# Kernel tuning notes

Hardware: AMD Instinct MI355X
Metric: run time of the kernel (lower is better)

## Reference

```python
import jax, jax.numpy as jnp
import numpy as np

B, T, D, H = 2, 2048, 2048, 16
HD = D // H
SCALE = HD ** -0.5
NEG_INF = float('-inf')


def setup_inputs() -> dict:
    key = jax.random.key(0)
    ks = jax.random.split(key, 10)
    x = jax.random.normal(ks[0], (B, T, D), dtype=jnp.float32)
    # causal float mask: 0 on/below diagonal, -inf above (broadcast over B, H)
    causal = jnp.triu(jnp.ones((T, T), dtype=bool), k=1)
    mask = jnp.where(causal, NEG_INF, 0.0).astype(jnp.float32)[None, None]
    # xavier_uniform for [D, D]: bound = sqrt(6 / (D + D))
    bound = float(np.sqrt(6.0 / (D + D)))
    def xav(k):
        return jax.random.uniform(k, (D, D), jnp.float32, -bound, bound)
    wq, wk, wv, wo = xav(ks[1]), xav(ks[2]), xav(ks[3]), xav(ks[4])
    # biases: uniform_[0,1)
    bq = jax.random.uniform(ks[5], (D,), jnp.float32)
    bk = jax.random.uniform(ks[6], (D,), jnp.float32)
    bv = jax.random.uniform(ks[7], (D,), jnp.float32)
    bo = jax.random.uniform(ks[8], (D,), jnp.float32)
    return {"x": x, "mask": mask, "wq": wq, "bq": bq, "wk": wk, "bk": bk,
            "wv": wv, "bv": bv, "wo": wo, "bo": bo}


def reference(x, mask, wq, bq, wk, bk, wv, bv, wo, bo):
    b, t, d = x.shape
    def split_heads(y):  # [B,T,D] -> [B,H,T,HD]
        return y.reshape(b, t, H, HD).transpose(0, 2, 1, 3)
    q = split_heads(x @ wq.T + bq)
    k = split_heads(x @ wk.T + bk)
    v = split_heads(x @ wv.T + bv)
    scores = jnp.einsum('bhqd,bhkd->bhqk', q, k) * SCALE
    scores = jnp.where(mask == NEG_INF, NEG_INF, scores)
    attn = jax.nn.softmax(scores, axis=-1)
    out = jnp.einsum('bhqk,bhkd->bhqd', attn, v)  # [B,H,T,HD]
    out = out.transpose(0, 2, 1, 3).reshape(b, t, d)
    return out @ wo.T + bo
```

## Files before the change

### kernel.cpp

```cpp
#include <hip/hip_runtime.h>

typedef unsigned short u16;
typedef __bf16 bf16x8 __attribute__((ext_vector_type(8)));
typedef float f32x4 __attribute__((ext_vector_type(4)));

constexpr int B_ = 2, T_ = 2048, D_ = 2048, H_ = 16, HD_ = 128;
constexpr int MROWS = B_ * T_;
constexpr int KD = D_;
constexpr int ND = D_;
#define SL2E (0.08838834764831845f * 1.4426950408889634f)

__device__ __forceinline__ u16 f2bf(float f) {
  unsigned u = __float_as_uint(f);
  u += 0x7FFF + ((u >> 16) & 1);
  return (u16)(u >> 16);
}

__device__ __forceinline__ float fexp2(float x) { return __builtin_amdgcn_exp2f(x); }

__device__ __forceinline__ void async16(const void* g, void* l) {
  __builtin_amdgcn_global_load_lds((__attribute__((address_space(1))) void*)g,
                                   (__attribute__((address_space(3))) void*)l,
                                   16, 0, 0);
}

__global__ void cvt6_kernel(const float* __restrict__ x,
                            const float* __restrict__ w0, const float* __restrict__ w1,
                            const float* __restrict__ w2, const float* __restrict__ w3,
                            u16* __restrict__ xo,
                            u16* __restrict__ o0, u16* __restrict__ o1,
                            u16* __restrict__ o2, u16* __restrict__ o3) {
  const int y = blockIdx.y;
  const float* in = y == 0 ? x : y == 1 ? x + 4194304 :
                    y == 2 ? w0 : y == 3 ? w1 : y == 4 ? w2 : w3;
  u16* out = y == 0 ? xo : y == 1 ? xo + 4194304 :
             y == 2 ? o0 : y == 3 ? o1 : y == 4 ? o2 : o3;
  const int i = (blockIdx.x * blockDim.x + threadIdx.x) * 4;
  const float4 v = *(const float4*)(in + i);
  ushort4 h;
  h.x = f2bf(v.x); h.y = f2bf(v.y); h.z = f2bf(v.z); h.w = f2bf(v.w);
  *(ushort4*)(out + i) = h;
}

template <int MODE>
__device__ __forceinline__ void gemm_body(const u16* __restrict__ A,
                                          const u16* __restrict__ Bw,
                                          const float* __restrict__ bias,
                                          void* __restrict__ outp,
                                          u16* As, u16* Bs) {
  constexpr int BK = 32;
  const int tid = threadIdx.x;
  const int wave = tid >> 6;
  const int lane = tid & 63;
  const int quad = lane >> 4;
  const int l16 = lane & 15;
  const int wm = (wave >> 1) * 64;
  const int wn = (wave & 1) * 64;
  const int mBase = blockIdx.y * 128;
  const int nBase = blockIdx.x * 128;

  f32x4 acc[4][4] = {};

  const int srow = wave * 32 + (lane >> 2);
  const int soff = ((lane & 3) ^ ((lane >> 3) & 3)) * 8;
  const u16* Ag = A + (size_t)(mBase + srow) * KD + soff;
  const u16* Bg = Bw + (size_t)(nBase + srow) * KD + soff;
  u16* AsW0 = &As[(wave * 32) * BK];
  u16* AsW1 = &As[(wave * 32 + 16) * BK];
  u16* BsW0 = &Bs[(wave * 32) * BK];
  u16* BsW1 = &Bs[(wave * 32 + 16) * BK];

  const int sw = (quad ^ ((l16 >> 1) & 3)) * 8;

  for (int k0 = 0; k0 < KD; k0 += BK) {
    __syncthreads();
    async16(Ag + k0, AsW0);
    async16(Ag + 16 * KD + k0, AsW1);
    async16(Bg + k0, BsW0);
    async16(Bg + 16 * KD + k0, BsW1);
    __syncthreads();

    bf16x8 a[4], b[4];
#pragma unroll
    for (int i = 0; i < 4; i++)
      a[i] = *(const bf16x8*)&As[(wm + i * 16 + l16) * BK + sw];
#pragma unroll
    for (int j = 0; j < 4; j++)
      b[j] = *(const bf16x8*)&Bs[(wn + j * 16 + l16) * BK + sw];
#pragma unroll
    for (int i = 0; i < 4; i++)
#pragma unroll
      for (int j = 0; j < 4; j++)
        acc[i][j] = __builtin_amdgcn_mfma_f32_16x16x32_bf16(a[i], b[j], acc[i][j], 0, 0, 0);
  }

  float* outF = (float*)outp;
  u16* outH = (u16*)outp;
#pragma unroll
  for (int i = 0; i < 4; i++) {
#pragma unroll
    for (int j = 0; j < 4; j++) {
      const int col = nBase + wn + j * 16 + l16;
      const float bv = bias[col];
#pragma unroll
      for (int r = 0; r < 4; r++) {
        const int row = mBase + wm + i * 16 + quad * 4 + r;
        const float v = acc[i][j][r] + bv;
        if (MODE == 0) {
          outH[(size_t)row * ND + col] = f2bf(v);
        } else if (MODE == 1) {
          const int bb = row >> 11;
          const int t = row & (T_ - 1);
          const int h = col >> 7;
          const int d = col & (HD_ - 1);
          outH[(size_t)(((bb * H_ + h) << 7) + d) * T_ + t] = f2bf(v);
        } else {
          outF[(size_t)row * ND + col] = v;
        }
      }
    }
  }
}

__global__ __launch_bounds__(256) void gemm_qkv(const u16* __restrict__ A,
                                                const u16* __restrict__ Wq, const u16* __restrict__ Wk,
                                                const u16* __restrict__ Wv,
                                                const float* __restrict__ bq, const float* __restrict__ bk,
                                                const float* __restrict__ bv,
                                                u16* __restrict__ Qo, u16* __restrict__ Ko,
                                                u16* __restrict__ Vo) {
  __shared__ u16 As[128 * 32];
  __shared__ u16 Bs[128 * 32];
  const int z = blockIdx.z;
  const u16* Bw = z == 0 ? Wq : z == 1 ? Wk : Wv;
  const float* bias = z == 0 ? bq : z == 1 ? bk : bv;
  if (z == 2)
    gemm_body<1>(A, Bw, bias, (void*)Vo, As, Bs);
  else
    gemm_body<0>(A, Bw, bias, (void*)(z == 0 ? Qo : Ko), As, Bs);
}

__global__ __launch_bounds__(256) void gemm_out(const u16* __restrict__ A, const u16* __restrict__ Bw,
                                                const float* __restrict__ bias, float* __restrict__ outp) {
  __shared__ u16 As[128 * 32];
  __shared__ u16 Bs[128 * 32];
  gemm_body<2>(A, Bw, bias, (void*)outp, As, Bs);
}

constexpr int PSTR = 72;

__global__ __launch_bounds__(256, 2) void attn_kernel(const u16* __restrict__ Q,
                                                      const u16* __restrict__ Kc,
                                                      const u16* __restrict__ Vt,
                                                      u16* __restrict__ O) {
  __shared__ u16 Ks[2][64 * 128];
  __shared__ u16 Vs[2][128 * 64];
  __shared__ u16 Ps[4 * 16 * PSTR];
  const int tid = threadIdx.x;
  const int wave = tid >> 6;
  const int lane = tid & 63;
  const int quad = lane >> 4;
  const int l16 = lane & 15;
  const int lo = blockIdx.x;
  const int hi = 31 - lo;
  const int bh = blockIdx.y;
  const int b = bh >> 4;
  const int h = bh & 15;

  const int tIdx[2] = {lo, hi};

  bf16x8 qf[2][4];
#pragma unroll
  for (int t = 0; t < 2; t++) {
    const u16* Qp = Q + (size_t)(b * T_ + tIdx[t] * 64 + wave * 16 + l16) * D_ + h * HD_;
#pragma unroll
    for (int kc = 0; kc < 4; kc++)
      qf[t][kc] = *(const bf16x8*)(Qp + kc * 32 + quad * 8);
  }

  f32x4 o[2][8] = {};
  float mrow[2], lrow[2];
#pragma unroll
  for (int t = 0; t < 2; t++) { mrow[t] = -__builtin_huge_valf(); lrow[t] = 0.f; }

  const u16* Kg = Kc + (size_t)(b * T_) * D_ + h * HD_;
  const u16* Vg = Vt + (size_t)((b * H_ + h) * HD_) * T_;
  u16* Pw = &Ps[wave * 16 * PSTR];
  const int swz = (l16 & 7);

  const u16* kgp[4];
  int klo[4];
  const u16* vgp[4];
  int vlo[4];
#pragma unroll
  for (int c = 0; c < 4; c++) {
    const int krl = wave * 16 + c * 4 + (lane >> 4);
    const int kch = (lane & 15) ^ (krl & 7);
    kgp[c] = Kg + (size_t)krl * D_ + kch * 8;
    klo[c] = (wave * 16 + c * 4) * 128;
    const int vrl = wave * 32 + c * 8 + (lane >> 3);
    const int vch = (lane & 7) ^ (vrl & 7);
    vgp[c] = Vg + (size_t)vrl * T_ + vch * 8;
    vlo[c] = (wave * 32 + c * 8) * 64;
  }

#pragma unroll
  for (int c = 0; c < 4; c++) async16(kgp[c], &Ks[0][klo[c]]);
#pragma unroll
  for (int c = 0; c < 4; c++) async16(vgp[c], &Vs[0][vlo[c]]);

  for (int kt = 0; kt <= hi; kt++) {
    const int cur = kt & 1;
    __syncthreads();

    if (kt < hi) {
      const int nxt = cur ^ 1;
#pragma unroll
      for (int c = 0; c < 4; c++) async16(kgp[c] + (size_t)(kt + 1) * 64 * D_, &Ks[nxt][klo[c]]);
#pragma unroll
      for (int c = 0; c < 4; c++) async16(vgp[c] + (size_t)(kt + 1) * 64, &Vs[nxt][vlo[c]]);
    }

#pragma unroll
    for (int t = 0; t < 2; t++) {
      if (t == 0 && kt > lo) continue;

      f32x4 st[4];
#pragma unroll
      for (int nt = 0; nt < 4; nt++) {
        f32x4 a = {};
#pragma unroll
        for (int kc = 0; kc < 4; kc++) {
          const int pos = (kc * 4 + quad) ^ swz;
          bf16x8 kf = *(const bf16x8*)&Ks[cur][(nt * 16 + l16) * 128 + pos * 8];
          a = __builtin_amdgcn_mfma_f32_16x16x32_bf16(kf, qf[t][kc], a, 0, 0, 0);
        }
        st[nt] = a;
      }

      const bool diag = (kt == tIdx[t]);
#pragma unroll
      for (int nt = 0; nt < 4; nt++)
#pragma unroll
        for (int r = 0; r < 4; r++) {
          float v = st[nt][r] * SL2E;
          if (diag) {
            const int kcol = nt * 16 + quad * 4 + r;
            const int qrow = wave * 16 + l16;
            if (kcol > qrow) v = -__builtin_huge_valf();
          }
          st[nt][r] = v;
        }

      float mx = st[0][0];
#pragma unroll
      for (int nt = 0; nt < 4; nt++)
#pragma unroll
        for (int r = 0; r < 4; r++) mx = fmaxf(mx, st[nt][r]);
      mx = fmaxf(mx, __shfl_xor(mx, 16));
      mx = fmaxf(mx, __shfl_xor(mx, 32));

      if (__all(mx - mrow[t] <= 8.0f)) {
        const float mold = mrow[t];
        float sum = 0.f;
#pragma unroll
        for (int nt = 0; nt < 4; nt++)
#pragma unroll
          for (int r = 0; r < 4; r++) {
            const float p = fexp2(st[nt][r] - mold);
            st[nt][r] = p;
            sum += p;
          }
        lrow[t] += sum;
      } else {
        const float mnew = fmaxf(mrow[t], mx);
        const float alpha = fexp2(mrow[t] - mnew);
        mrow[t] = mnew;
        float sum = 0.f;
#pragma unroll
        for (int nt = 0; nt < 4; nt++)
#pragma unroll
          for (int r = 0; r < 4; r++) {
            const float p = fexp2(st[nt][r] - mnew);
            st[nt][r] = p;
            sum += p;
          }
        lrow[t] = lrow[t] * alpha + sum;

        float af[4];
#pragma unroll
        for (int r = 0; r < 4; r++) af[r] = __shfl(alpha, quad * 4 + r);
#pragma unroll
        for (int dt = 0; dt < 8; dt++)
#pragma unroll
          for (int r = 0; r < 4; r++)
            o[t][dt][r] *= af[r];
      }

#pragma unroll
      for (int nt = 0; nt < 4; nt++) {
        ushort4 pk;
        pk.x = f2bf(st[nt][0]); pk.y = f2bf(st[nt][1]);
        pk.z = f2bf(st[nt][2]); pk.w = f2bf(st[nt][3]);
        *(ushort4*)&Pw[l16 * PSTR + nt * 16 + quad * 4] = pk;
      }

      bf16x8 pf[2];
#pragma unroll
      for (int kc = 0; kc < 2; kc++)
        pf[kc] = *(const bf16x8*)&Pw[l16 * PSTR + kc * 32 + quad * 8];
#pragma unroll
      for (int dt = 0; dt < 8; dt++) {
#pragma unroll
        for (int kc = 0; kc < 2; kc++) {
          const int pos = (kc * 4 + quad) ^ swz;
          bf16x8 vf = *(const bf16x8*)&Vs[cur][(dt * 16 + l16) * 64 + pos * 8];
          o[t][dt] = __builtin_amdgcn_mfma_f32_16x16x32_bf16(pf[kc], vf, o[t][dt], 0, 0, 0);
        }
      }
    }
  }

#pragma unroll
  for (int t = 0; t < 2; t++) {
    float ltot = lrow[t];
    ltot += __shfl_xor(ltot, 16);
    ltot += __shfl_xor(ltot, 32);
    float linv[4];
#pragma unroll
    for (int r = 0; r < 4; r++) linv[r] = 1.f / __shfl(ltot, quad * 4 + r);
#pragma unroll
    for (int dt = 0; dt < 8; dt++)
#pragma unroll
      for (int r = 0; r < 4; r++) {
        const int rowg = b * T_ + tIdx[t] * 64 + wave * 16 + quad * 4 + r;
        const int col = h * HD_ + dt * 16 + l16;
        O[(size_t)rowg * D_ + col] = f2bf(o[t][dt][r] * linv[r]);
      }
  }
}

extern "C" void kernel_launch(void* const* d_in, const int* in_sizes, int n_in,
                              void* d_out, int out_size, void* d_ws, size_t ws_size,
                              hipStream_t stream) {
  (void)in_sizes; (void)n_in; (void)out_size; (void)ws_size;
  const float* x  = (const float*)d_in[0];
  const float* wq = (const float*)d_in[2];
  const float* bq = (const float*)d_in[3];
  const float* wk = (const float*)d_in[4];
  const float* bk = (const float*)d_in[5];
  const float* wv = (const float*)d_in[6];
  const float* bv = (const float*)d_in[7];
  const float* wo = (const float*)d_in[8];
  const float* bo = (const float*)d_in[9];

  u16* ws  = (u16*)d_ws;
  u16* xb  = ws;
  u16* wqb = ws + 8388608;
  u16* wkb = ws + 12582912;
  u16* wvb = ws + 16777216;
  u16* wob = ws + 20971520;
  u16* Qb  = ws + 25165824;
  u16* Kb  = ws + 33554432;
  u16* Vtb = ws + 41943040;
  u16* Ob  = ws + 50331648;

  cvt6_kernel<<<dim3(4096, 6), 256, 0, stream>>>(x, wq, wk, wv, wo,
                                                 xb, wqb, wkb, wvb, wob);

  dim3 gg(ND / 128, MROWS / 128, 3);
  gemm_qkv<<<gg, 256, 0, stream>>>(xb, wqb, wkb, wvb, bq, bk, bv, Qb, Kb, Vtb);
  attn_kernel<<<dim3(16, B_ * H_), 256, 0, stream>>>(Qb, Kb, Vtb, Ob);
  gemm_out<<<dim3(ND / 128, MROWS / 128), 256, 0, stream>>>(Ob, wob, bo, (float*)d_out);
}
```

Measured before the change: 391.1 us.

## Assign contiguous 128-row query tiles per block and share K/V fragments

Replaces the balanced lo/hi pairing of two 64-row query tiles with one contiguous 128-row query tile per block. Each wave now handles two 16-row query groups against the same K and V fragments, so each LDS fragment load feeds two MFMAs. The block loops over 2p+2 key tiles and masks causally by absolute position on the last two. This roughly halves K/V traffic per block, but the work per block becomes uneven. Blocks range from 2 to 32 key tiles, each doing two groups, so the longest block may run longer than under the old balanced pairing.

```diff
diff --git a/kernel.cpp b/kernel.cpp
--- a/kernel.cpp
+++ b/kernel.cpp
@@ -161,27 +161,25 @@
   const int lane = tid & 63;
   const int quad = lane >> 4;
   const int l16 = lane & 15;
-  const int lo = blockIdx.x;
-  const int hi = 31 - lo;
+  const int p = 15 - blockIdx.x;
   const int bh = blockIdx.y;
   const int b = bh >> 4;
   const int h = bh & 15;
-
-  const int tIdx[2] = {lo, hi};
+  const int nkt = 2 * p + 2;
 
   bf16x8 qf[2][4];
 #pragma unroll
-  for (int t = 0; t < 2; t++) {
-    const u16* Qp = Q + (size_t)(b * T_ + tIdx[t] * 64 + wave * 16 + l16) * D_ + h * HD_;
+  for (int qg = 0; qg < 2; qg++) {
+    const u16* Qp = Q + (size_t)(b * T_ + p * 128 + wave * 32 + qg * 16 + l16) * D_ + h * HD_;
 #pragma unroll
     for (int kc = 0; kc < 4; kc++)
-      qf[t][kc] = *(const bf16x8*)(Qp + kc * 32 + quad * 8);
+      qf[qg][kc] = *(const bf16x8*)(Qp + kc * 32 + quad * 8);
   }
 
   f32x4 o[2][8] = {};
   float mrow[2], lrow[2];
 #pragma unroll
-  for (int t = 0; t < 2; t++) { mrow[t] = -__builtin_huge_valf(); lrow[t] = 0.f; }
+  for (int qg = 0; qg < 2; qg++) { mrow[qg] = -__builtin_huge_valf(); lrow[qg] = 0.f; }
 
   const u16* Kg = Kc + (size_t)(b * T_) * D_ + h * HD_;
   const u16* Vg = Vt + (size_t)((b * H_ + h) * HD_) * T_;
@@ -209,11 +207,11 @@
 #pragma unroll
   for (int c = 0; c < 4; c++) async16(vgp[c], &Vs[0][vlo[c]]);
 
-  for (int kt = 0; kt <= hi; kt++) {
+  for (int kt = 0; kt < nkt; kt++) {
     const int cur = kt & 1;
     __syncthreads();
 
-    if (kt < hi) {
+    if (kt + 1 < nkt) {
       const int nxt = cur ^ 1;
 #pragma unroll
       for (int c = 0; c < 4; c++) async16(kgp[c] + (size_t)(kt + 1) * 64 * D_, &Ks[nxt][klo[c]]);
@@ -221,71 +219,77 @@
       for (int c = 0; c < 4; c++) async16(vgp[c] + (size_t)(kt + 1) * 64, &Vs[nxt][vlo[c]]);
     }
 
-#pragma unroll
-    for (int t = 0; t < 2; t++) {
-      if (t == 0 && kt > lo) continue;
-
-      f32x4 st[4];
-#pragma unroll
-      for (int nt = 0; nt < 4; nt++) {
-        f32x4 a = {};
-#pragma unroll
-        for (int kc = 0; kc < 4; kc++) {
-          const int pos = (kc * 4 + quad) ^ swz;
-          bf16x8 kf = *(const bf16x8*)&Ks[cur][(nt * 16 + l16) * 128 + pos * 8];
-          a = __builtin_amdgcn_mfma_f32_16x16x32_bf16(kf, qf[t][kc], a, 0, 0, 0);
-        }
-        st[nt] = a;
-      }
-
-      const bool diag = (kt == tIdx[t]);
+    f32x4 st[2][4];
+#pragma unroll
+    for (int nt = 0; nt < 4; nt++) {
+      bf16x8 kf[4];
+#pragma unroll
+      for (int kc = 0; kc < 4; kc++) {
+        const int pos = (kc * 4 + quad) ^ swz;
+        kf[kc] = *(const bf16x8*)&Ks[cur][(nt * 16 + l16) * 128 + pos * 8];
+      }
+      f32x4 a0 = {}, a1 = {};
+#pragma unroll
+      for (int kc = 0; kc < 4; kc++)
+        a0 = __builtin_amdgcn_mfma_f32_16x16x32_bf16(kf[kc], qf[0][kc], a0, 0, 0, 0);
+#pragma unroll
+      for (int kc = 0; kc < 4; kc++)
+        a1 = __builtin_amdgcn_mfma_f32_16x16x32_bf16(kf[kc], qf[1][kc], a1, 0, 0, 0);
+      st[0][nt] = a0;
+      st[1][nt] = a1;
+    }
+
+    const bool diag = (kt >= 2 * p);
+    bf16x8 pf[2][2];
+#pragma unroll
+    for (int qg = 0; qg < 2; qg++) {
 #pragma unroll
       for (int nt = 0; nt < 4; nt++)
 #pragma unroll
         for (int r = 0; r < 4; r++) {
-          float v = st[nt][r] * SL2E;
+          float v = st[qg][nt][r] * SL2E;
           if (diag) {
-            const int kcol = nt * 16 + quad * 4 + r;
-            const int qrow = wave * 16 + l16;
+            const int kcol = kt * 64 + nt * 16 + quad * 4 + r;
+            const int qrow = p * 128 + wave * 32 + qg * 16 + l16;
             if (kcol > qrow) v = -__builtin_huge_valf();
           }
-          st[nt][r] = v;
+          st[qg][nt][r] = v;
         }
 
-      float mx = st[0][0];
+      float mx = st[qg][0][0];
 #pragma unroll
       for (int nt = 0; nt < 4; nt++)
 #pragma unroll
-        for (int r = 0; r < 4; r++) mx = fmaxf(mx, st[nt][r]);
+        for (int r = 0; r < 4; r++) mx = fmaxf(mx, st[qg][nt][r]);
       mx = fmaxf(mx, __shfl_xor(mx, 16));
       mx = fmaxf(mx, __shfl_xor(mx, 32));
 
-      if (__all(mx - mrow[t] <= 8.0f)) {
-        const float mold = mrow[t];
+      if (__all(mx - mrow[qg] <= 8.0f)) {
+        const float mold = mrow[qg];
         float sum = 0.f;
 #pragma unroll
         for (int nt = 0; nt < 4; nt++)
 #pragma unroll
           for (int r = 0; r < 4; r++) {
-            const float p = fexp2(st[nt][r] - mold);
-            st[nt][r] = p;
-            sum += p;
+            const float pv = fexp2(st[qg][nt][r] - mold);
+            st[qg][nt][r] = pv;
+            sum += pv;
           }
-        lrow[t] += sum;
+        lrow[qg] += sum;
       } else {
-        const float mnew = fmaxf(mrow[t], mx);
-        const float alpha = fexp2(mrow[t] - mnew);
-        mrow[t] = mnew;
+        const float mnew = fmaxf(mrow[qg], mx);
+        const float alpha = fexp2(mrow[qg] - mnew);
+        mrow[qg] = mnew;
         float sum = 0.f;
 #pragma unroll
         for (int nt = 0; nt < 4; nt++)
 #pragma unroll
           for (int r = 0; r < 4; r++) {
-            const float p = fexp2(st[nt][r] - mnew);
-            st[nt][r] = p;
-            sum += p;
+            const float pv = fexp2(st[qg][nt][r] - mnew);
+            st[qg][nt][r] = pv;
+            sum += pv;
           }
-        lrow[t] = lrow[t] * alpha + sum;
+        lrow[qg] = lrow[qg] * alpha + sum;
 
         float af[4];
 #pragma unroll
@@ -294,36 +298,36 @@
         for (int dt = 0; dt < 8; dt++)
 #pragma unroll
           for (int r = 0; r < 4; r++)
-            o[t][dt][r] *= af[r];
+            o[qg][dt][r] *= af[r];
       }
 
 #pragma unroll
       for (int nt = 0; nt < 4; nt++) {
         ushort4 pk;
-        pk.x = f2bf(st[nt][0]); pk.y = f2bf(st[nt][1]);
-        pk.z = f2bf(st[nt][2]); pk.w = f2bf(st[nt][3]);
+        pk.x = f2bf(st[qg][nt][0]); pk.y = f2bf(st[qg][nt][1]);
+        pk.z = f2bf(st[qg][nt][2]); pk.w = f2bf(st[qg][nt][3]);
         *(ushort4*)&Pw[l16 * PSTR + nt * 16 + quad * 4] = pk;
       }
-
-      bf16x8 pf[2];
 #pragma unroll
       for (int kc = 0; kc < 2; kc++)
-        pf[kc] = *(const bf16x8*)&Pw[l16 * PSTR + kc * 32 + quad * 8];
-#pragma unroll
-      for (int dt = 0; dt < 8; dt++) {
-#pragma unroll
-        for (int kc = 0; kc < 2; kc++) {
-          const int pos = (kc * 4 + quad) ^ swz;
-          bf16x8 vf = *(const bf16x8*)&Vs[cur][(dt * 16 + l16) * 64 + pos * 8];
-          o[t][dt] = __builtin_amdgcn_mfma_f32_16x16x32_bf16(pf[kc], vf, o[t][dt], 0, 0, 0);
-        }
-      }
-    }
-  }
-
-#pragma unroll
-  for (int t = 0; t < 2; t++) {
-    float ltot = lrow[t];
+        pf[qg][kc] = *(const bf16x8*)&Pw[l16 * PSTR + kc * 32 + quad * 8];
+    }
+
+#pragma unroll
+    for (int dt = 0; dt < 8; dt++) {
+#pragma unroll
+      for (int kc = 0; kc < 2; kc++) {
+        const int pos = (kc * 4 + quad) ^ swz;
+        bf16x8 vf = *(const bf16x8*)&Vs[cur][(dt * 16 + l16) * 64 + pos * 8];
+        o[0][dt] = __builtin_amdgcn_mfma_f32_16x16x32_bf16(pf[0][kc], vf, o[0][dt], 0, 0, 0);
+        o[1][dt] = __builtin_amdgcn_mfma_f32_16x16x32_bf16(pf[1][kc], vf, o[1][dt], 0, 0, 0);
+      }
+    }
+  }
+
+#pragma unroll
+  for (int qg = 0; qg < 2; qg++) {
+    float ltot = lrow[qg];
     ltot += __shfl_xor(ltot, 16);
     ltot += __shfl_xor(ltot, 32);
     float linv[4];
@@ -333,9 +337,9 @@
     for (int dt = 0; dt < 8; dt++)
 #pragma unroll
       for (int r = 0; r < 4; r++) {
-        const int rowg = b * T_ + tIdx[t] * 64 + wave * 16 + quad * 4 + r;
+        const int rowg = b * T_ + p * 128 + wave * 32 + qg * 16 + quad * 4 + r;
         const int col = h * HD_ + dt * 16 + l16;
-        O[(size_t)rowg * D_ + col] = f2bf(o[t][dt][r] * linv[r]);
+        O[(size_t)rowg * D_ + col] = f2bf(o[qg][dt][r] * linv[r]);
       }
   }
 }
```

Result: slower. 415.4 us (+6.2%).
